# Kernel tuning notes

Measured on AMD Instinct MI355X. Metric: run time of the kernel, lower is better.

The kernel has to match this reference:

```python
import jax, jax.numpy as jnp
from jax import lax
import numpy as np

SHAPE = (50, 60, 65)   # -> after net: (17, 27, 32), flatten = 14688
NEG = 0.01             # LeakyReLU default slope
B, N = 8, 80000        # batch size, total active voxels


def _lrelu(x):
    return jnp.where(x >= 0, x, NEG * x)


def _sparse_conv(x, w, b, m):
    # Regular (non-submanifold) sparse conv == dense VALID conv on densified
    # input (inactive sites are 0 so they contribute nothing). Output site is
    # active iff any input site in the kernel footprint is active; bias is
    # added only at active output sites.
    k = w.shape[2]
    y = lax.conv_general_dilated(x, w, (1, 1, 1), 'VALID',
                                 dimension_numbers=('NCDHW', 'OIDHW', 'NCDHW'))
    m2 = lax.reduce_window(m, 0.0, lax.max, (1, 1, k, k, k), (1, 1, 1, 1, 1), 'VALID')
    y = jnp.where(m2 > 0, y + b[None, :, None, None, None], 0.0)
    return y, m2


def _sparse_maxpool(x, m, k):
    # spconv SparseMaxPool: max over ACTIVE sites only (inactive excluded, not 0)
    xm = jnp.where(m > 0, x, -jnp.inf)
    p = lax.reduce_window(xm, -jnp.inf, lax.max, (1, 1, k, k, k), (1, 1, 1, 1, 1), 'VALID')
    m2 = lax.reduce_window(m, 0.0, lax.max, (1, 1, k, k, k), (1, 1, 1, 1, 1), 'VALID')
    return jnp.where(m2 > 0, p, 0.0), m2


def setup_inputs() -> dict:
    key = jax.random.key(0)
    ks = jax.random.split(key, 24)
    D, H, W = SHAPE
    features = jax.random.normal(ks[0], (N, 1), dtype=jnp.float32)
    bi = jax.random.randint(ks[1], (N,), 0, B)
    zi = jax.random.randint(ks[2], (N,), 0, D)
    yi = jax.random.randint(ks[3], (N,), 0, H)
    xi = jax.random.randint(ks[4], (N,), 0, W)
    coors = jnp.stack([bi, zi, yi, xi], axis=1).astype(jnp.int32)
    s = 0.05
    p = {}
    p['w1'] = jax.random.normal(ks[5], (32, 1, 4, 4, 4), jnp.float32) * s
    p['b1'] = jax.random.normal(ks[6], (32,), jnp.float32) * s
    p['w2'] = jax.random.normal(ks[7], (32, 32, 4, 4, 4), jnp.float32) * s
    p['b2'] = jax.random.normal(ks[8], (32,), jnp.float32) * s
    p['w3'] = jax.random.normal(ks[9], (32, 32, 4, 4, 4), jnp.float32) * s
    p['b3'] = jax.random.normal(ks[10], (32,), jnp.float32) * s
    p['w4'] = jax.random.normal(ks[11], (32, 32, 4, 4, 4), jnp.float32) * s
    p['b4'] = jax.random.normal(ks[12], (32,), jnp.float32) * s
    p['w5'] = jax.random.normal(ks[13], (32, 32, 4, 4, 4), jnp.float32) * s
    p['b5'] = jax.random.normal(ks[14], (32,), jnp.float32) * s
    p['w6'] = jax.random.normal(ks[15], (32, 32, 4, 4, 4), jnp.float32) * s
    p['b6'] = jax.random.normal(ks[16], (32,), jnp.float32) * s
    p['w7'] = jax.random.normal(ks[17], (1, 32, 4, 4, 4), jnp.float32) * s
    p['b7'] = jax.random.normal(ks[18], (1,), jnp.float32) * s
    p['W8'] = jax.random.normal(ks[19], (14688, 1000), jnp.float32) * 0.01
    p['b8'] = jax.random.normal(ks[20], (1000,), jnp.float32) * s
    p['W9'] = jax.random.normal(ks[21], (1000, 1000), jnp.float32) * 0.03
    p['b9'] = jax.random.normal(ks[22], (1000,), jnp.float32) * s
    p['W10'] = jax.random.normal(ks[23], (1000, 1), jnp.float32) * 0.03
    p['b10'] = jnp.zeros((1,), jnp.float32)
    return dict(features=features, coors=coors, batch_size=B, **p)


def reference(features, coors, batch_size,
              w1, b1, w2, b2, w3, b3, w4, b4, w5, b5, w6, b6, w7, b7,
              W8, b8, W9, b9, W10, b10):
    D, H, W = SHAPE
    bi, zi, yi, xi = coors[:, 0], coors[:, 1], coors[:, 2], coors[:, 3]
    dense = jnp.zeros((batch_size, 1, D, H, W), features.dtype)
    dense = dense.at[bi, 0, zi, yi, xi].set(features[:, 0])
    mask = jnp.zeros((batch_size, 1, D, H, W), features.dtype)
    mask = mask.at[bi, 0, zi, yi, xi].set(1.0)

    x, m = _sparse_conv(dense, w1, b1, mask); x = _lrelu(x)
    x, m = _sparse_conv(x, w2, b2, m);        x = _lrelu(x)
    x, m = _sparse_maxpool(x, m, 5)
    x, m = _sparse_conv(x, w3, b3, m);        x = _lrelu(x)
    x, m = _sparse_conv(x, w4, b4, m);        x = _lrelu(x)
    x, m = _sparse_maxpool(x, m, 5)
    x, m = _sparse_conv(x, w5, b5, m);        x = _lrelu(x)
    x, m = _sparse_conv(x, w6, b6, m);        x = _lrelu(x)
    x, m = _sparse_conv(x, w7, b7, m);        x = _lrelu(x)
    x, m = _sparse_maxpool(x, m, 5)

    # ToDense (inactive sites already 0) + Flatten -> [B, 14688]
    h = x.reshape(x.shape[0], -1)
    h = _lrelu(h @ W8 + b8)
    h = _lrelu(h @ W9 + b9)
    out = _lrelu(h @ W10 + b10)
    return out
```

## Files before the change

kernel.cpp:

```cpp
#include <hip/hip_runtime.h>
#include <cstddef>


#define NEGSLOPE 0.01f
#define NINF (-3.0e38f)

#define TZ 4
#define TY 4
#define TXT 16
#define IZ 7
#define IY 7
#define IX 19
#define NV (IZ*IY*IX)

typedef __attribute__((ext_vector_type(8)))  short    short8;
typedef __attribute__((ext_vector_type(4)))  unsigned uint4v;
typedef __attribute__((ext_vector_type(16))) float    floatx16;

constexpr int ilog2c(int v) { return v == 1 ? 0 : 1 + ilog2c(v / 2); }

__device__ __forceinline__ float lrelu(float v) { return v >= 0.f ? v : NEGSLOPE * v; }

__device__ __forceinline__ unsigned short f2bf(float f) {
  unsigned b = __float_as_uint(f);
  return (unsigned short)((b + 0x7fffu + ((b >> 16) & 1u)) >> 16);
}
__device__ __forceinline__ float bf2f(unsigned short h) {
  return __uint_as_float(((unsigned)h) << 16);
}
__device__ __forceinline__ unsigned splitpair(float a, float b, unsigned& lo) {
  unsigned short ha = f2bf(a), hb = f2bf(b);
  unsigned short la = f2bf(a - bf2f(ha)), lb = f2bf(b - bf2f(hb));
  lo = (unsigned)la | ((unsigned)lb << 16);
  return (unsigned)ha | ((unsigned)hb << 16);
}

__device__ __forceinline__ short8 ld_frag(const uint2* s2, int v, int oct) {
  uint2 u0 = s2[v * 5 + oct * 2];
  uint2 u1 = s2[v * 5 + oct * 2 + 1];
  uint4v t; t.x = u0.x; t.y = u0.y; t.z = u1.x; t.w = u1.y;
  return __builtin_bit_cast(short8, t);
}

__global__ void k_claim(const int* __restrict__ coors, unsigned* __restrict__ claim, int N) {
  int i = blockIdx.x * blockDim.x + threadIdx.x;
  if (i >= N) return;
  int b = coors[4*i], z = coors[4*i+1], y = coors[4*i+2], x = coors[4*i+3];
  int v = ((b*50 + z)*60 + y)*65 + x;
  atomicMax(&claim[v], (unsigned)(i + 1));
}

__global__ void k_scatter(const int* __restrict__ coors, const float* __restrict__ feat,
                          const unsigned* __restrict__ claim,
                          float* __restrict__ x0, float* __restrict__ m0, int N) {
  int i = blockIdx.x * blockDim.x + threadIdx.x;
  if (i >= N) return;
  int b = coors[4*i], z = coors[4*i+1], y = coors[4*i+2], x = coors[4*i+3];
  int v = ((b*50 + z)*60 + y)*65 + x;
  m0[v] = 1.f;
  if (claim[v] == (unsigned)(i + 1)) x0[v] = feat[i];
}

__global__ void k_repack(const float* __restrict__ w, float* __restrict__ wr, int CI, int CO) {
  int i = blockIdx.x * blockDim.x + threadIdx.x;
  int tot = CO * CI * 64;
  if (i >= tot) return;
  int k = i & 63;
  int ci = (i >> 6) % CI;
  int co = i / (64 * CI);
  wr[(k * CI + ci) * CO + co] = w[i];
}

__global__ void k_repack_mfma5(const float* __restrict__ wA, const float* __restrict__ wB,
                               const float* __restrict__ wC, const float* __restrict__ wD,
                               const float* __restrict__ wE, unsigned short* __restrict__ tbl0) {
  int layer = blockIdx.y;
  const float* w = layer == 0 ? wA : layer == 1 ? wB : layer == 2 ? wC
                 : layer == 3 ? wD : wE;
  unsigned short* tbl = tbl0 + (size_t)layer * 262144;
  int i = blockIdx.x * blockDim.x + threadIdx.x;
  if (i >= 64*4*2*64) return;
  int lane = i & 63; int t = i >> 6;
  int pack = t & 1; t >>= 1;
  int pass = t & 3; int tap = t >> 2;
  int co = lane & 31; int oct = lane >> 5;
#pragma unroll
  for (int j = 0; j < 8; ++j) {
    int k = oct * 8 + j;
    int ci = pass * 8 + (k & 7);
    int part = ((k >> 3) ^ pack) & 1;
    float wv = w[((co * 32 + ci) << 6) + tap];
    unsigned short wh = f2bf(wv);
    unsigned short r = part ? f2bf(wv - bf2f(wh)) : wh;
    tbl[(size_t)i * 8 + j] = r;
  }
}

template<int K>
__global__ __launch_bounds__(256, 4)
void kd_fused(const float* __restrict__ in, float* __restrict__ out,
              int Zi, int Yi, int Xi, int Zo, int Yo, int Xo,
              int tilesZ, int tilesY, int tilesX) {
  constexpr int TDZ = 4, TDY = 8, TDX = 32;
  constexpr int HZ = TDZ + K - 1, HY = TDY + K - 1, HX = TDX + K - 1;
  __shared__ float sA[HZ * HY * HX];
  __shared__ float sB[TDZ * HY * HX];
  __shared__ float sC[TDZ * TDY * HX];
  int bid = blockIdx.x;
  int txi = bid % tilesX; bid /= tilesX;
  int tyi = bid % tilesY; bid /= tilesY;
  int tzi = bid % tilesZ; int item = bid / tilesZ;
  const int z0 = tzi * TDZ, y0 = tyi * TDY, x0 = txi * TDX;
  const int tid = threadIdx.x;
  const float* ib = in + (size_t)item * Zi * Yi * Xi;

  for (int idx = tid; idx < HZ * HY * HX; idx += 256) {
    int iz = idx / (HY * HX); int r = idx - iz * (HY * HX);
    int iy = r / HX; int ix = r - iy * HX;
    int gz = z0 + iz, gy = y0 + iy, gx = x0 + ix;
    float v = 0.f;
    if (gz < Zi && gy < Yi && gx < Xi) v = ib[((size_t)gz * Yi + gy) * Xi + gx];
    sA[idx] = v;
  }
  __syncthreads();
  for (int idx = tid; idx < TDZ * HY * HX; idx += 256) {
    int z = idx / (HY * HX); int r = idx - z * (HY * HX);
    float m = 0.f;
#pragma unroll
    for (int d = 0; d < K; ++d) m = fmaxf(m, sA[(z + d) * (HY * HX) + r]);
    sB[idx] = m;
  }
  __syncthreads();
  for (int idx = tid; idx < TDZ * TDY * HX; idx += 256) {
    int z = idx / (TDY * HX); int r = idx - z * (TDY * HX);
    int y = r / HX; int x = r - y * HX;
    float m = 0.f;
#pragma unroll
    for (int d = 0; d < K; ++d) m = fmaxf(m, sB[z * (HY * HX) + (y + d) * HX + x]);
    sC[idx] = m;
  }
  __syncthreads();
  const int perOut = Zo * Yo * Xo;
  for (int idx = tid; idx < TDZ * TDY * TDX; idx += 256) {
    int z = idx / (TDY * TDX); int r = idx - z * (TDY * TDX);
    int y = r / TDX; int x = r - y * TDX;
    int gz = z0 + z, gy = y0 + y, gx = x0 + x;
    if (gz < Zo && gy < Yo && gx < Xo) {
      float m = 0.f;
#pragma unroll
      for (int d = 0; d < K; ++d) m = fmaxf(m, sC[z * (TDY * HX) + y * HX + x + d]);
      out[(size_t)item * perOut + ((size_t)gz * Yo + gy) * Xo + gx] = m;
    }
  }
}

template<int TZL, int TYL, int TXL, int IZL, int IYL, int IXL, bool POOLOUT>
__global__ __launch_bounds__(256, 4)
void k_conv32m(const float* __restrict__ in, const unsigned short* __restrict__ tbl,
               const float* __restrict__ bias, const float* __restrict__ mo,
               float* __restrict__ out,
               int Zi, int Yi, int Xi, int Zo, int Yo, int Xo,
               int tilesZ, int tilesY, int tilesX) {
  constexpr int NVL = IZL * IYL * IXL;
  constexpr int LXs = ilog2c(TXL);
  constexpr int LYs = ilog2c(TYL);
  __shared__ unsigned sU[NVL * 10];
  const int perIn = Zi * Yi * Xi;
  const int perOut = Zo * Yo * Xo;
  int bid = blockIdx.x;
  int txi = bid % tilesX; bid /= tilesX;
  int tyi = bid % tilesY; bid /= tilesY;
  int tzi = bid % tilesZ; int item = bid / tilesZ;
  const int z0 = tzi * TZL, y0 = tyi * TYL, x0 = txi * TXL;
  const int tid = threadIdx.x;
  const int lane = tid & 63;
  const int col = lane & 31;
  const int oct = lane >> 5;
  const int wv  = tid >> 6;

  int lvBase0, lvBase1;
  {
    int vt0 = (2*wv + 0)*32 + col;
    int vt1 = (2*wv + 1)*32 + col;
    lvBase0 = ((vt0 >> (LXs+LYs))*IYL + ((vt0 >> LXs) & (TYL-1)))*IXL + (vt0 & (TXL-1));
    lvBase1 = ((vt1 >> (LXs+LYs))*IYL + ((vt1 >> LXs) & (TYL-1)))*IXL + (vt1 & (TXL-1));
  }

  floatx16 acc0, acc1;
#pragma unroll
  for (int r = 0; r < 16; ++r) { acc0[r] = 0.f; acc1[r] = 0.f; }

  const float* inb = in + (size_t)item * perIn * 32;
  const char* tb = (const char*)tbl + lane * 16;
  uint2* s2 = (uint2*)sU;

#pragma unroll 1
  for (int p = 0; p < 4; ++p) {
    __syncthreads();
    for (int idx = tid; idx < NVL; idx += 256) {
      int iz = idx / (IYL * IXL); int r = idx - iz * (IYL * IXL);
      int iy = r / IXL; int ix = r - iy * IXL;
      int gz = z0 + iz, gy = y0 + iy, gx = x0 + ix;
      float4 f0 = make_float4(0.f,0.f,0.f,0.f), f1 = make_float4(0.f,0.f,0.f,0.f);
      if (gz < Zi && gy < Yi && gx < Xi) {
        const float* vp = inb + (size_t)((gz * Yi + gy) * Xi + gx) * 32 + p * 8;
        f0 = *(const float4*)vp;
        f1 = *(const float4*)(vp + 4);
      }
      unsigned l0, l1, l2, l3;
      unsigned h0 = splitpair(f0.x, f0.y, l0);
      unsigned h1 = splitpair(f0.z, f0.w, l1);
      unsigned h2 = splitpair(f1.x, f1.y, l2);
      unsigned h3 = splitpair(f1.z, f1.w, l3);
      s2[idx * 5 + 0] = make_uint2(h0, h1);
      s2[idx * 5 + 1] = make_uint2(h2, h3);
      s2[idx * 5 + 2] = make_uint2(l0, l1);
      s2[idx * 5 + 3] = make_uint2(l2, l3);
    }
    __syncthreads();

    const char* tp = tb + (size_t)p * 2048;
    short8 b0 = *(const short8*)(tp);
    short8 b1 = *(const short8*)(tp + 1024);
#pragma unroll 2
    for (int tap = 0; tap < 64; ++tap) {
      int nt = tap < 63 ? tap + 1 : 63;
      short8 nb0 = *(const short8*)(tp + (size_t)nt * 8192);
      short8 nb1 = *(const short8*)(tp + (size_t)nt * 8192 + 1024);
      int kz = tap >> 4, ky = (tap >> 2) & 3, kx = tap & 3;
      int sOff = (kz * IYL + ky) * IXL + kx;
      short8 a0 = ld_frag(s2, lvBase0 + sOff, oct);
      short8 a1 = ld_frag(s2, lvBase1 + sOff, oct);
      acc0 = __builtin_amdgcn_mfma_f32_32x32x16_bf16(a0, b0, acc0, 0, 0, 0);
      acc0 = __builtin_amdgcn_mfma_f32_32x32x16_bf16(a0, b1, acc0, 0, 0, 0);
      acc1 = __builtin_amdgcn_mfma_f32_32x32x16_bf16(a1, b0, acc1, 0, 0, 0);
      acc1 = __builtin_amdgcn_mfma_f32_32x32x16_bf16(a1, b1, acc1, 0, 0, 0);
      b0 = nb0; b1 = nb1;
    }
  }

  const float bco = bias[col];
#pragma unroll
  for (int gg = 0; gg < 2; ++gg) {
    int vtb = (2*wv + gg) * 32;
#pragma unroll
    for (int rg = 0; rg < 16; ++rg) {
      int row = (rg & 3) + 8 * (rg >> 2) + 4 * oct;
      int vt = vtb + row;
      int oz = vt >> (LXs+LYs), oy = (vt >> LXs) & (TYL-1), ox = vt & (TXL-1);
      int gz = z0 + oz, gy = y0 + oy, gx = x0 + ox;
      if (gz < Zo && gy < Yo && gx < Xo) {
        int ov = item * perOut + (gz * Yo + gy) * Xo + gx;
        float val = (gg == 0) ? acc0[rg] : acc1[rg];
        bool act = mo[ov] > 0.f;
        float vv = act ? lrelu(val + bco) : (POOLOUT ? NINF : 0.f);
        out[(size_t)ov * 32 + col] = vv;
      }
    }
  }
}

template<int TZL, int TYL, int TXL, int IZL, int IYL, int IXL, bool POOLOUT>
static void launch_conv32(hipStream_t stream,
                          const float* in, const unsigned short* tbl, const float* bias,
                          const float* mo, float* o,
                          int Zi, int Yi, int Xi, int Zo, int Yo, int Xo, int nI) {
  int tz = (Zo + TZL - 1) / TZL, ty = (Yo + TYL - 1) / TYL, tx = (Xo + TXL - 1) / TXL;
  k_conv32m<TZL,TYL,TXL,IZL,IYL,IXL,POOLOUT><<<nI * tz * ty * tx, 256, 0, stream>>>(
      in, tbl, bias, mo, o, Zi, Yi, Xi, Zo, Yo, Xo, tz, ty, tx);
}

__global__ __launch_bounds__(256, 4)
void k_conv1t(const float* __restrict__ in, const float* __restrict__ wr,
              const float* __restrict__ bias, const float* __restrict__ mo,
              float* __restrict__ out,
              int Zi, int Yi, int Xi, int Zo, int Yo, int Xo,
              int tilesZ, int tilesY, int tilesX) {
  __shared__ float sinf[NV];
  __shared__ float4 wsh[512];
  {
    const float4* wr4 = (const float4*)wr;
    for (int idx = threadIdx.x; idx < 512; idx += 256) wsh[idx] = wr4[idx];
  }
  const int perIn = Zi * Yi * Xi;
  const int perOut = Zo * Yo * Xo;
  int bid = blockIdx.x;
  int txi = bid % tilesX; bid /= tilesX;
  int tyi = bid % tilesY; bid /= tilesY;
  int tzi = bid % tilesZ; int item = bid / tilesZ;
  const int z0 = tzi * TZ, y0 = tyi * TY, x0 = txi * TXT;
  const int tid = threadIdx.x;
  const int ox = tid & 15, oy = (tid >> 4) & 3, oz = tid >> 6;

  const float* inb = in + (size_t)item * perIn;
  for (int idx = tid; idx < NV; idx += 256) {
    int iz = idx / (IY * IX); int r = idx - iz * (IY * IX);
    int iy = r / IX; int ix = r - iy * IX;
    int gz = z0 + iz, gy = y0 + iy, gx = x0 + ix;
    float val = 0.f;
    if (gz < Zi && gy < Yi && gx < Xi)
      val = inb[(size_t)((gz * Yi + gy) * Xi + gx)];
    sinf[idx] = val;
  }
  __syncthreads();

  float4 acc[8];
#pragma unroll
  for (int j = 0; j < 8; ++j) acc[j] = make_float4(0.f, 0.f, 0.f, 0.f);

#pragma unroll 1
  for (int tap = 0; tap < 64; ++tap) {
    int kz = tap >> 4, ky = (tap >> 2) & 3, kx = tap & 3;
    int lv = ((oz + kz) * IY + (oy + ky)) * IX + (ox + kx);
    float av = sinf[lv];
#pragma unroll
    for (int j = 0; j < 8; ++j) {
      float4 wvv = wsh[tap * 8 + j];
      acc[j].x = fmaf(av, wvv.x, acc[j].x);
      acc[j].y = fmaf(av, wvv.y, acc[j].y);
      acc[j].z = fmaf(av, wvv.z, acc[j].z);
      acc[j].w = fmaf(av, wvv.w, acc[j].w);
    }
  }

  int gz = z0 + oz, gy = y0 + oy, gx = x0 + ox;
  if (gz < Zo && gy < Yo && gx < Xo) {
    int ov = item * perOut + (gz * Yo + gy) * Xo + gx;
    bool act = mo[ov] > 0.f;
    const float4* b4 = (const float4*)bias;
    float* op = out + (size_t)ov * 32;
#pragma unroll
    for (int j = 0; j < 8; ++j) {
      float4 r = acc[j]; float4 bj = b4[j];
      r.x = lrelu(act ? (r.x + bj.x) : 0.f);
      r.y = lrelu(act ? (r.y + bj.y) : 0.f);
      r.z = lrelu(act ? (r.z + bj.z) : 0.f);
      r.w = lrelu(act ? (r.w + bj.w) : 0.f);
      *(float4*)(op + j * 4) = r;
    }
  }
}

__global__ __launch_bounds__(256, 2)
void k_conv7t(const float* __restrict__ in, const float* __restrict__ wr,
              const float* __restrict__ bias, const float* __restrict__ mo,
              float* __restrict__ out,
              int Zi, int Yi, int Xi, int Zo, int Yo, int Xo,
              int tilesZ, int tilesY, int tilesX) {
  __shared__ float4 sin4[4][NV];
  __shared__ float4 wsh[512];
  {
    const float4* wr4 = (const float4*)wr;
    for (int idx = threadIdx.x; idx < 512; idx += 256) wsh[idx] = wr4[idx];
  }
  const int perIn = Zi * Yi * Xi;
  const int perOut = Zo * Yo * Xo;
  int bid = blockIdx.x;
  int txi = bid % tilesX; bid /= tilesX;
  int tyi = bid % tilesY; bid /= tilesY;
  int tzi = bid % tilesZ; int item = bid / tilesZ;
  const int z0 = tzi * TZ, y0 = tyi * TY, x0 = txi * TXT;
  const int tid = threadIdx.x;
  const int ox = tid & 15, oy = (tid >> 4) & 3, oz = tid >> 6;

  const float* inb = in + (size_t)item * perIn * 32;
  float acc = 0.f;

#pragma unroll 1
  for (int h = 0; h < 2; ++h) {
    __syncthreads();
    for (int idx = tid; idx < NV * 4; idx += 256) {
      int q = idx / NV; int v = idx - q * NV;
      int iz = v / (IY * IX); int r = v - iz * (IY * IX);
      int iy = r / IX; int ix = r - iy * IX;
      int gz = z0 + iz, gy = y0 + iy, gx = x0 + ix;
      float4 val = make_float4(0.f, 0.f, 0.f, 0.f);
      if (gz < Zi && gy < Yi && gx < Xi)
        val = *(const float4*)(inb + (size_t)((gz * Yi + gy) * Xi + gx) * 32 + h * 16 + q * 4);
      sin4[q][v] = val;
    }
    __syncthreads();
#pragma unroll 1
    for (int tap = 0; tap < 64; ++tap) {
      int kz = tap >> 4, ky = (tap >> 2) & 3, kx = tap & 3;
      int lv = ((oz + kz) * IY + (oy + ky)) * IX + (ox + kx);
      float4 a0 = sin4[0][lv];
      float4 a1 = sin4[1][lv];
      float4 a2 = sin4[2][lv];
      float4 a3 = sin4[3][lv];
      float4 w0 = wsh[tap * 8 + h * 4 + 0];
      float4 w1 = wsh[tap * 8 + h * 4 + 1];
      float4 w2 = wsh[tap * 8 + h * 4 + 2];
      float4 w3 = wsh[tap * 8 + h * 4 + 3];
      acc += a0.x*w0.x + a0.y*w0.y + a0.z*w0.z + a0.w*w0.w
           + a1.x*w1.x + a1.y*w1.y + a1.z*w1.z + a1.w*w1.w
           + a2.x*w2.x + a2.y*w2.y + a2.z*w2.z + a2.w*w2.w
           + a3.x*w3.x + a3.y*w3.y + a3.z*w3.z + a3.w*w3.w;
    }
  }

  int gz = z0 + oz, gy = y0 + oy, gx = x0 + ox;
  if (gz < Zo && gy < Yo && gx < Xo) {
    int ov = item * perOut + (gz * Yo + gy) * Xo + gx;
    bool act = mo[ov] > 0.f;
    out[ov] = act ? lrelu(acc + bias[0]) : NINF;
  }
}

__global__ void k_pool_z(const float* __restrict__ in, float* __restrict__ out,
                         int Zi, int Yi, int Xi, int Zo, int nI) {
  int gid = blockIdx.x * blockDim.x + threadIdx.x;
  int perOut = Zo * Yi * Xi;
  int tot = nI * perOut * 8;
  if (gid >= tot) return;
  int c4 = gid & 7; int v = gid >> 3;
  int item = v / perOut;
  int r = v - item * perOut;
  int x = r % Xi; int t = r / Xi;
  int y = t % Yi; int z = t / Yi;
  int ib = item * Zi * Yi * Xi;
  float4 acc = {NINF, NINF, NINF, NINF};
  for (int j = 0; j < 5; j++) {
    int vi = ib + ((z + j)*Yi + y)*Xi + x;
    float4 val = *(const float4*)(in + (size_t)vi*32 + c4*4);
    acc.x = fmaxf(acc.x, val.x); acc.y = fmaxf(acc.y, val.y);
    acc.z = fmaxf(acc.z, val.z); acc.w = fmaxf(acc.w, val.w);
  }
  *(float4*)(out + (size_t)v*32 + c4*4) = acc;
}

__global__ void k_pool_yx(const float* __restrict__ in, const float* __restrict__ mp,
                          float* __restrict__ out,
                          int Z, int Yi, int Xi, int Yo, int Xo, int nI) {
  int gid = blockIdx.x * blockDim.x + threadIdx.x;
  int runsX = (Xo + 3) >> 2;
  int perR = Z * Yo * runsX;
  int tot = nI * perR * 8;
  if (gid >= tot) return;
  int c4 = gid & 7; int r = gid >> 3;
  int item = r / perR;
  int rr = r - item * perR;
  int xr = rr % runsX; int t = rr / runsX;
  int y = t % Yo; int z = t / Yo;
  int x0 = xr << 2;
  const float* ib = in + (size_t)item * Z * Yi * Xi * 32;

  float4 ym[8];
#pragma unroll
  for (int dx = 0; dx < 8; ++dx) ym[dx] = make_float4(NINF, NINF, NINF, NINF);
#pragma unroll
  for (int dy = 0; dy < 5; ++dy) {
    const float* rowb = ib + (size_t)((z * Yi + y + dy) * Xi) * 32;
#pragma unroll
    for (int dx = 0; dx < 8; ++dx) {
      int xx = x0 + dx;
      if (xx < Xi) {
        float4 v = *(const float4*)(rowb + (size_t)xx * 32 + c4 * 4);
        ym[dx].x = fmaxf(ym[dx].x, v.x); ym[dx].y = fmaxf(ym[dx].y, v.y);
        ym[dx].z = fmaxf(ym[dx].z, v.z); ym[dx].w = fmaxf(ym[dx].w, v.w);
      }
    }
  }
  int perOut = Z * Yo * Xo;
#pragma unroll
  for (int j = 0; j < 4; ++j) {
    int xx = x0 + j;
    if (xx < Xo) {
      float4 a = ym[j];
#pragma unroll
      for (int d = 1; d < 5; ++d) {
        a.x = fmaxf(a.x, ym[j+d].x); a.y = fmaxf(a.y, ym[j+d].y);
        a.z = fmaxf(a.z, ym[j+d].z); a.w = fmaxf(a.w, ym[j+d].w);
      }
      int v = item * perOut + (z * Yo + y) * Xo + xx;
      bool act = mp[v] > 0.f;
      float4 rrv;
      rrv.x = act ? a.x : 0.f; rrv.y = act ? a.y : 0.f;
      rrv.z = act ? a.z : 0.f; rrv.w = act ? a.w : 0.f;
      *(float4*)(out + (size_t)v*32 + c4*4) = rrv;
    }
  }
}

__global__ void k_pool3(const float* __restrict__ xin,
                        const float* __restrict__ mp, float* __restrict__ out, int nI) {
  int gid = blockIdx.x * blockDim.x + threadIdx.x;
  int perOut = 17 * 27 * 32;
  int tot = nI * perOut;
  if (gid >= tot) return;
  int item = gid / perOut;
  int r = gid - item * perOut;
  int x = r & 31; int t = r >> 5;
  int y = t % 27; int z = t / 27;
  const float* xb = xin + (size_t)item * 23436;
  float acc = NINF;
  for (int dz = 0; dz < 5; dz++)
    for (int dy = 0; dy < 5; dy++) {
      const float* rowx = xb + (size_t)(((z + dz)*31 + y + dy)*36 + x);
      for (int dx = 0; dx < 5; dx++)
        acc = fmaxf(acc, rowx[dx]);
    }
  out[gid] = (mp[gid] > 0.f) ? acc : 0.f;
}

__global__ __launch_bounds__(256, 4)
void k_fc_part(const float* __restrict__ X, const float* __restrict__ Wm,
               float* __restrict__ part, int K, int Ncol, int Kc) {
  __shared__ float sm[16][16][8];
  int ks = blockIdx.y;
  int k0 = ks * Kc;
  int k1 = k0 + Kc; if (k1 > K) k1 = K;
  int cl = threadIdx.x & 15;
  int kt = threadIdx.x >> 4;
  int col = blockIdx.x * 16 + cl;
  float a0=0.f,a1=0.f,a2=0.f,a3=0.f,a4=0.f,a5=0.f,a6=0.f,a7=0.f;
  if (col < Ncol) {
    for (int k = k0 + kt; k < k1; k += 16) {
      float w = Wm[(size_t)k * Ncol + col];
      a0 += X[0 * K + k] * w; a1 += X[1 * K + k] * w;
      a2 += X[2 * K + k] * w; a3 += X[3 * K + k] * w;
      a4 += X[4 * K + k] * w; a5 += X[5 * K + k] * w;
      a6 += X[6 * K + k] * w; a7 += X[7 * K + k] * w;
    }
  }
  sm[kt][cl][0]=a0; sm[kt][cl][1]=a1; sm[kt][cl][2]=a2; sm[kt][cl][3]=a3;
  sm[kt][cl][4]=a4; sm[kt][cl][5]=a5; sm[kt][cl][6]=a6; sm[kt][cl][7]=a7;
  __syncthreads();
  if (threadIdx.x < 128) {
    int c = threadIdx.x & 15;
    int b = threadIdx.x >> 4;
    float s = 0.f;
#pragma unroll
    for (int k = 0; k < 16; k++) s += sm[k][c][b];
    int cc = blockIdx.x * 16 + c;
    if (cc < Ncol) part[((size_t)ks * 8 + b) * Ncol + cc] = s;
  }
}

__global__ void k_fc_fin(const float* __restrict__ part, int ns,
                         const float* __restrict__ bias, float* __restrict__ out, int Ncol) {
  int i = blockIdx.x * blockDim.x + threadIdx.x;
  if (i >= 8 * Ncol) return;
  int b = i / Ncol;
  int c = i - b * Ncol;
  float s = 0.f;
  for (int ks = 0; ks < ns; ks++) s += part[((size_t)ks * 8 + b) * Ncol + c];
  out[i] = lrelu(s + bias[c]);
}

__global__ __launch_bounds__(256, 4)
void k_fc(const float* __restrict__ X, const float* __restrict__ Wm,
          const float* __restrict__ bias, float* __restrict__ out,
          int K, int Ncol) {
  __shared__ float sm[16][16][8];
  int cl = threadIdx.x & 15;
  int kt = threadIdx.x >> 4;
  int col = blockIdx.x * 16 + cl;
  float a0=0.f,a1=0.f,a2=0.f,a3=0.f,a4=0.f,a5=0.f,a6=0.f,a7=0.f;
  if (col < Ncol) {
    for (int k = kt; k < K; k += 16) {
      float w = Wm[(size_t)k * Ncol + col];
      a0 += X[0 * K + k] * w; a1 += X[1 * K + k] * w;
      a2 += X[2 * K + k] * w; a3 += X[3 * K + k] * w;
      a4 += X[4 * K + k] * w; a5 += X[5 * K + k] * w;
      a6 += X[6 * K + k] * w; a7 += X[7 * K + k] * w;
    }
  }
  sm[kt][cl][0]=a0; sm[kt][cl][1]=a1; sm[kt][cl][2]=a2; sm[kt][cl][3]=a3;
  sm[kt][cl][4]=a4; sm[kt][cl][5]=a5; sm[kt][cl][6]=a6; sm[kt][cl][7]=a7;
  __syncthreads();
  if (threadIdx.x < 128) {
    int c = threadIdx.x & 15;
    int b = threadIdx.x >> 4;
    float s = 0.f;
#pragma unroll
    for (int k = 0; k < 16; k++) s += sm[k][c][b];
    int cc = blockIdx.x * 16 + c;
    if (cc < Ncol) out[b * Ncol + cc] = lrelu(s + bias[cc]);
  }
}

static inline int G256(long long n) { return (int)((n + 255) / 256); }

extern "C" void kernel_launch(void* const* d_in, const int* in_sizes, int n_in,
                              void* d_out, int out_size, void* d_ws, size_t ws_size,
                              hipStream_t stream) {
  const float* feat  = (const float*)d_in[0];
  const int*   coors = (const int*)d_in[1];
  const float* w1 = (const float*)d_in[3];  const float* b1 = (const float*)d_in[4];
  const float* w2 = (const float*)d_in[5];  const float* b2 = (const float*)d_in[6];
  const float* w3 = (const float*)d_in[7];  const float* b3 = (const float*)d_in[8];
  const float* w4 = (const float*)d_in[9];  const float* b4 = (const float*)d_in[10];
  const float* w5 = (const float*)d_in[11]; const float* b5 = (const float*)d_in[12];
  const float* w6 = (const float*)d_in[13]; const float* b6 = (const float*)d_in[14];
  const float* w7 = (const float*)d_in[15]; const float* b7 = (const float*)d_in[16];
  const float* W8 = (const float*)d_in[17]; const float* b8 = (const float*)d_in[18];
  const float* W9 = (const float*)d_in[19]; const float* b9 = (const float*)d_in[20];
  const float* W10= (const float*)d_in[21]; const float* b10= (const float*)d_in[22];
  float* out = (float*)d_out;

  char* ws = (char*)d_ws;
  size_t off = 0;
  auto alloc = [&](size_t nfloats) -> float* {
    float* p = (float*)(ws + off);
    off += ((nfloats * 4 + 1023) / 1024) * 1024;
    return p;
  };

  float* x0  = alloc(1560000);
  float* m0  = alloc(1560000);
  float* m1  = alloc(8 * 166098);
  float* m2  = alloc(8 * 140184);
  float* mp1 = alloc(8 * 110000);
  float* m3  = alloc(8 * 90428);
  float* m4  = alloc(8 * 73304);
  float* mp2 = alloc(8 * 54000);
  float* m5  = alloc(8 * 41958);
  float* m6  = alloc(8 * 31824);
  float* m7  = alloc(8 * 23436);
  float* mp3 = alloc(8 * 14688);
  float* p3  = alloc(8 * 14688);
  float* wr1 = alloc(2048);
  float* wr7 = alloc(2048);
  unsigned short* tb2 = (unsigned short*)alloc(131072);
  unsigned short* tb3 = (unsigned short*)alloc(131072);
  unsigned short* tb4 = (unsigned short*)alloc(131072);
  unsigned short* tb5 = (unsigned short*)alloc(131072);
  unsigned short* tb6 = (unsigned short*)alloc(131072);
  float* part= alloc(64000);
  float* h8  = alloc(8000);
  float* h9  = alloc(8000);
  size_t fixedOff = off;

  const size_t perItemAB = ((size_t)5315136*4 + 1023)/1024*1024
                         + ((size_t)4485888*4 + 1023)/1024*1024
                         + ((size_t)23436*4 + 1023)/1024*1024;
  int G = 0;
  for (int g : {8, 4, 2, 1})
    if (fixedOff + (size_t)g * perItemAB <= ws_size) { G = g; break; }
  if (G == 0) return;

  float* A  = alloc((size_t)G * 5315136);
  float* Bb = alloc((size_t)G * 4485888);
  float* x7 = alloc((size_t)G * 23436);
  unsigned* claim = (unsigned*)A;

  hipMemsetAsync(claim, 0, 1560000 * 4, stream);
  hipMemsetAsync(x0,    0, 1560000 * 4, stream);
  hipMemsetAsync(m0,    0, 1560000 * 4, stream);

  k_repack<<<G256(32*1*64),  256, 0, stream>>>(w1, wr1, 1, 32);
  k_repack<<<G256(1*32*64),  256, 0, stream>>>(w7, wr7, 32, 1);
  k_repack_mfma5<<<dim3(128, 5), 256, 0, stream>>>(w2, w3, w4, w5, w6, tb2);

  const int N = 80000;
  k_claim  <<<G256(N), 256, 0, stream>>>(coors, claim, N);
  k_scatter<<<G256(N), 256, 0, stream>>>(coors, feat, claim, x0, m0, N);

  auto dil3 = [&](const float* src, float* dst,
                  int Zi, int Yi, int Xi, int Zo, int Yo, int Xo, int K) {
    int tz = (Zo + 3) / 4, ty = (Yo + 7) / 8, tx = (Xo + 31) / 32;
    if (K == 4)
      kd_fused<4><<<8 * tz * ty * tx, 256, 0, stream>>>(src, dst, Zi,Yi,Xi, Zo,Yo,Xo, tz,ty,tx);
    else
      kd_fused<5><<<8 * tz * ty * tx, 256, 0, stream>>>(src, dst, Zi,Yi,Xi, Zo,Yo,Xo, tz,ty,tx);
  };
  dil3(m0,  m1,  50,60,65, 47,57,62, 4);
  dil3(m1,  m2,  47,57,62, 44,54,59, 4);
  dil3(m2,  mp1, 44,54,59, 40,50,55, 5);
  dil3(mp1, m3,  40,50,55, 37,47,52, 4);
  dil3(m3,  m4,  37,47,52, 34,44,49, 4);
  dil3(m4,  mp2, 34,44,49, 30,40,45, 5);
  dil3(mp2, m5,  30,40,45, 27,37,42, 4);
  dil3(m5,  m6,  27,37,42, 24,34,39, 4);
  dil3(m6,  m7,  24,34,39, 21,31,36, 4);
  dil3(m7,  mp3, 21,31,36, 17,27,32, 5);

  for (int g0 = 0; g0 < 8; g0 += G) {
    const float* x0g  = x0  + (size_t)g0 * 195000;
    const float* m1g  = m1  + (size_t)g0 * 166098;
    const float* m2g  = m2  + (size_t)g0 * 140184;
    const float* mp1g = mp1 + (size_t)g0 * 110000;
    const float* m3g  = m3  + (size_t)g0 * 90428;
    const float* m4g  = m4  + (size_t)g0 * 73304;
    const float* mp2g = mp2 + (size_t)g0 * 54000;
    const float* m5g  = m5  + (size_t)g0 * 41958;
    const float* m6g  = m6  + (size_t)g0 * 31824;
    const float* m7g  = m7  + (size_t)g0 * 23436;
    const float* mp3g = mp3 + (size_t)g0 * 14688;

    {
      int tz = (47 + TZ - 1) / TZ, ty = (57 + TY - 1) / TY, tx = (62 + TXT - 1) / TXT;
      k_conv1t<<<G * tz * ty * tx, 256, 0, stream>>>(
          x0g, wr1, b1, m1g, A, 50,60,65, 47,57,62, tz, ty, tx);
    }
    launch_conv32<4,4,16,7,7,19,true>(stream, A, tb2, b2, m2g, Bb, 47,57,62, 44,54,59, G);
    k_pool_z<<<G256((long long)G*127440*8), 256, 0, stream>>>(Bb, A, 44,54,59, 40, G);
    k_pool_yx<<<G256((long long)G*40*50*14*8), 256, 0, stream>>>(A, mp1g, Bb, 40,54,59, 50,55, G);
    launch_conv32<8,8,4,11,11,7,false>(stream, Bb, tb3, b3, m3g, A, 40,50,55, 37,47,52, G);
    launch_conv32<4,16,4,7,19,7,true>(stream, A, tb4, b4, m4g, Bb, 37,47,52, 34,44,49, G);
    k_pool_z<<<G256((long long)G*64680*8), 256, 0, stream>>>(Bb, A, 34,44,49, 30, G);
    k_pool_yx<<<G256((long long)G*30*40*12*8), 256, 0, stream>>>(A, mp2g, Bb, 30,44,49, 40,45, G);
    launch_conv32<4,4,16,7,7,19,false>(stream, Bb, tb5, b5, m5g, A, 30,40,45, 27,37,42, G);
    launch_conv32<8,4,8,11,7,11,false>(stream, A, tb6, b6, m6g, Bb, 27,37,42, 24,34,39, G);
    {
      int tz = (21 + TZ - 1) / TZ, ty = (31 + TY - 1) / TY, tx = (36 + TXT - 1) / TXT;
      k_conv7t<<<G * tz * ty * tx, 256, 0, stream>>>(
          Bb, wr7, b7, m7g, x7, 24,34,39, 21,31,36, tz, ty, tx);
    }
    k_pool3<<<G256((long long)G*14688), 256, 0, stream>>>(
        x7, mp3g, p3 + (size_t)g0 * 14688, G);
  }

  k_fc_part<<<dim3(63, 8), 256, 0, stream>>>(p3, W8, part, 14688, 1000, 1836);
  k_fc_fin <<<G256(8000), 256, 0, stream>>>(part, 8, b8, h8, 1000);
  k_fc_part<<<dim3(63, 4), 256, 0, stream>>>(h8, W9, part, 1000, 1000, 250);
  k_fc_fin <<<G256(8000), 256, 0, stream>>>(part, 4, b9, h9, 1000);
  k_fc<<<1, 256, 0, stream>>>(h9, W10, b10, out, 1000, 1);
}
```

Baseline: 3.106 ms.

## Use sliding-window z-pool, drop B-fragment prefetch, relax conv1 launch bounds

Replaces the per-output z max-pool with a kernel in which each thread walks a chunk of PCZ output depths along a column, keeping a sliding window of four loaded values so each input is read about once instead of five times. Separately, the MFMA conv loop stops software-prefetching the next tap's weight fragments and loads them inline, and k_conv1t's launch bounds drop from 4 to 2 blocks per CU. The pooling change cuts redundant global reads but launches fewer threads. Removing the prefetch may expose load latency, and the relaxed launch bounds trade occupancy for more registers.

After: 2.991 ms. 3.7% less time.

```diff
diff --git a/kernel.cpp b/kernel.cpp
--- a/kernel.cpp
+++ b/kernel.cpp
@@ -13,6 +13,8 @@
 #define IX 19
 #define NV (IZ*IY*IX)
 
+#define PCZ 10
+
 typedef __attribute__((ext_vector_type(8)))  short    short8;
 typedef __attribute__((ext_vector_type(4)))  unsigned uint4v;
 typedef __attribute__((ext_vector_type(16))) float    floatx16;
@@ -33,6 +35,13 @@
   unsigned short la = f2bf(a - bf2f(ha)), lb = f2bf(b - bf2f(hb));
   lo = (unsigned)la | ((unsigned)lb << 16);
   return (unsigned)ha | ((unsigned)hb << 16);
+}
+
+__device__ __forceinline__ float4 max4(float4 a, float4 b) {
+  float4 r;
+  r.x = fmaxf(a.x, b.x); r.y = fmaxf(a.y, b.y);
+  r.z = fmaxf(a.z, b.z); r.w = fmaxf(a.w, b.w);
+  return r;
 }
 
 __device__ __forceinline__ short8 ld_frag(const uint2* s2, int v, int oct) {
@@ -220,22 +229,18 @@
     __syncthreads();
 
     const char* tp = tb + (size_t)p * 2048;
-    short8 b0 = *(const short8*)(tp);
-    short8 b1 = *(const short8*)(tp + 1024);
 #pragma unroll 2
     for (int tap = 0; tap < 64; ++tap) {
-      int nt = tap < 63 ? tap + 1 : 63;
-      short8 nb0 = *(const short8*)(tp + (size_t)nt * 8192);
-      short8 nb1 = *(const short8*)(tp + (size_t)nt * 8192 + 1024);
       int kz = tap >> 4, ky = (tap >> 2) & 3, kx = tap & 3;
       int sOff = (kz * IYL + ky) * IXL + kx;
+      short8 b0 = *(const short8*)(tp + (size_t)tap * 8192);
+      short8 b1 = *(const short8*)(tp + (size_t)tap * 8192 + 1024);
       short8 a0 = ld_frag(s2, lvBase0 + sOff, oct);
       short8 a1 = ld_frag(s2, lvBase1 + sOff, oct);
       acc0 = __builtin_amdgcn_mfma_f32_32x32x16_bf16(a0, b0, acc0, 0, 0, 0);
       acc0 = __builtin_amdgcn_mfma_f32_32x32x16_bf16(a0, b1, acc0, 0, 0, 0);
       acc1 = __builtin_amdgcn_mfma_f32_32x32x16_bf16(a1, b0, acc1, 0, 0, 0);
       acc1 = __builtin_amdgcn_mfma_f32_32x32x16_bf16(a1, b1, acc1, 0, 0, 0);
-      b0 = nb0; b1 = nb1;
     }
   }
 
@@ -270,7 +275,7 @@
       in, tbl, bias, mo, o, Zi, Yi, Xi, Zo, Yo, Xo, tz, ty, tx);
 }
 
-__global__ __launch_bounds__(256, 4)
+__global__ __launch_bounds__(256, 2)
 void k_conv1t(const float* __restrict__ in, const float* __restrict__ wr,
               const float* __restrict__ bias, const float* __restrict__ mo,
               float* __restrict__ out,
@@ -407,26 +412,34 @@
   }
 }
 
-__global__ void k_pool_z(const float* __restrict__ in, float* __restrict__ out,
-                         int Zi, int Yi, int Xi, int Zo, int nI) {
+__global__ void k_pool_zw(const float* __restrict__ in, float* __restrict__ out,
+                          int Zi, int Yi, int Xi, int Zo, int nI) {
   int gid = blockIdx.x * blockDim.x + threadIdx.x;
-  int perOut = Zo * Yi * Xi;
-  int tot = nI * perOut * 8;
-  if (gid >= tot) return;
-  int c4 = gid & 7; int v = gid >> 3;
-  int item = v / perOut;
-  int r = v - item * perOut;
-  int x = r % Xi; int t = r / Xi;
-  int y = t % Yi; int z = t / Yi;
-  int ib = item * Zi * Yi * Xi;
-  float4 acc = {NINF, NINF, NINF, NINF};
-  for (int j = 0; j < 5; j++) {
-    int vi = ib + ((z + j)*Yi + y)*Xi + x;
-    float4 val = *(const float4*)(in + (size_t)vi*32 + c4*4);
-    acc.x = fmaxf(acc.x, val.x); acc.y = fmaxf(acc.y, val.y);
-    acc.z = fmaxf(acc.z, val.z); acc.w = fmaxf(acc.w, val.w);
-  }
-  *(float4*)(out + (size_t)v*32 + c4*4) = acc;
+  int nCh = (Zo + PCZ - 1) / PCZ;
+  int perI = nCh * Yi * Xi * 8;
+  if (gid >= nI * perI) return;
+  int c4 = gid & 7; int t = gid >> 3;
+  int x = t % Xi; t /= Xi;
+  int y = t % Yi; t /= Yi;
+  int ch = t % nCh; int item = t / nCh;
+  int z0 = ch * PCZ;
+  int zend = z0 + PCZ; if (zend > Zo) zend = Zo;
+
+  const float* colp = in + ((size_t)((item * Zi) * Yi + y) * Xi + x) * 32 + c4 * 4;
+  const size_t zs = (size_t)Yi * Xi * 32;
+  float* ocolp = out + ((size_t)((item * Zo) * Yi + y) * Xi + x) * 32 + c4 * 4;
+
+  float4 w0 = *(const float4*)(colp + (size_t)(z0 + 0) * zs);
+  float4 w1 = *(const float4*)(colp + (size_t)(z0 + 1) * zs);
+  float4 w2 = *(const float4*)(colp + (size_t)(z0 + 2) * zs);
+  float4 w3 = *(const float4*)(colp + (size_t)(z0 + 3) * zs);
+#pragma unroll 2
+  for (int z = z0; z < zend; ++z) {
+    float4 c = *(const float4*)(colp + (size_t)(z + 4) * zs);
+    float4 m = max4(max4(w0, w1), max4(w2, max4(w3, c)));
+    *(float4*)(ocolp + (size_t)z * zs) = m;
+    w0 = w1; w1 = w2; w2 = w3; w3 = c;
+  }
 }
 
 __global__ void k_pool_yx(const float* __restrict__ in, const float* __restrict__ mp,
@@ -456,8 +469,7 @@
       int xx = x0 + dx;
       if (xx < Xi) {
         float4 v = *(const float4*)(rowb + (size_t)xx * 32 + c4 * 4);
-        ym[dx].x = fmaxf(ym[dx].x, v.x); ym[dx].y = fmaxf(ym[dx].y, v.y);
-        ym[dx].z = fmaxf(ym[dx].z, v.z); ym[dx].w = fmaxf(ym[dx].w, v.w);
+        ym[dx] = max4(ym[dx], v);
       }
     }
   }
@@ -468,10 +480,7 @@
     if (xx < Xo) {
       float4 a = ym[j];
 #pragma unroll
-      for (int d = 1; d < 5; ++d) {
-        a.x = fmaxf(a.x, ym[j+d].x); a.y = fmaxf(a.y, ym[j+d].y);
-        a.z = fmaxf(a.z, ym[j+d].z); a.w = fmaxf(a.w, ym[j+d].w);
-      }
+      for (int d = 1; d < 5; ++d) a = max4(a, ym[j + d]);
       int v = item * perOut + (z * Yo + y) * Xo + xx;
       bool act = mp[v] > 0.f;
       float4 rrv;
@@ -695,11 +704,17 @@
           x0g, wr1, b1, m1g, A, 50,60,65, 47,57,62, tz, ty, tx);
     }
     launch_conv32<4,4,16,7,7,19,true>(stream, A, tb2, b2, m2g, Bb, 47,57,62, 44,54,59, G);
-    k_pool_z<<<G256((long long)G*127440*8), 256, 0, stream>>>(Bb, A, 44,54,59, 40, G);
+    {
+      int nCh = (40 + PCZ - 1) / PCZ;
+      k_pool_zw<<<G256((long long)G * nCh * 54 * 59 * 8), 256, 0, stream>>>(Bb, A, 44,54,59, 40, G);
+    }
     k_pool_yx<<<G256((long long)G*40*50*14*8), 256, 0, stream>>>(A, mp1g, Bb, 40,54,59, 50,55, G);
     launch_conv32<8,8,4,11,11,7,false>(stream, Bb, tb3, b3, m3g, A, 40,50,55, 37,47,52, G);
     launch_conv32<4,16,4,7,19,7,true>(stream, A, tb4, b4, m4g, Bb, 37,47,52, 34,44,49, G);
-    k_pool_z<<<G256((long long)G*64680*8), 256, 0, stream>>>(Bb, A, 34,44,49, 30, G);
+    {
+      int nCh = (30 + PCZ - 1) / PCZ;
+      k_pool_zw<<<G256((long long)G * nCh * 44 * 49 * 8), 256, 0, stream>>>(Bb, A, 34,44,49, 30, G);
+    }
     k_pool_yx<<<G256((long long)G*30*40*12*8), 256, 0, stream>>>(A, mp2g, Bb, 30,44,49, 40,45, G);
     launch_conv32<4,4,16,7,7,19,false>(stream, Bb, tb5, b5, m5g, A, 30,40,45, 27,37,42, G);
     launch_conv32<8,4,8,11,7,11,false>(stream, A, tb6, b6, m6g, Bb, 27,37,42, 24,34,39, G);
```
